# Optimization experiments

Measured on AMD Instinct MI355X. Metric: run time of the kernel, lower is better.

The kernel has to match this reference:

```python
import jax, jax.numpy as jnp
import numpy as np

N, M, E, D = 20000, 1024, 640000, 256


def setup_inputs() -> dict:
    key = jax.random.key(0)
    ks = jax.random.split(key, 24)
    mask = jax.random.uniform(ks[0], (N, M)) < 0.05
    init = jnp.where(mask, jax.random.uniform(ks[1], (N, M), minval=0.1, maxval=1.0), 0.0)
    inp = {
        'init': init,
        'ei_cc': jax.random.randint(ks[2], (2, E), 0, N, dtype=jnp.int32),
        'ei_cac': jax.random.randint(ks[3], (2, E), 0, N, dtype=jnp.int32),
        'ei_csc': jax.random.randint(ks[4], (2, E), 0, N, dtype=jnp.int32),
        'ea_cc': jax.random.uniform(ks[5], (E,), minval=0.1, maxval=1.0),
        'ea_cac': jax.random.uniform(ks[6], (E,), minval=0.1, maxval=1.0),
        'ea_csc': jax.random.uniform(ks[7], (E,), minval=0.1, maxval=1.0),
        # Projection MLP: Linear(1,16) -> ReLU -> Linear(16,D)
        'pW1': jax.random.normal(ks[8], (1, 16)) * 0.5,
        'pb1': jnp.zeros((16,)),
        'pW2': jax.random.normal(ks[9], (16, D)) * 0.1,
        'pb2': jnp.zeros((D,)),
        # three GCN branches, 3 layers each (all D->D)
        'W_cc': jax.random.normal(ks[10], (3, D, D)) * 0.05,
        'b_cc': jnp.zeros((3, D)),
        'W_cac': jax.random.normal(ks[11], (3, D, D)) * 0.05,
        'b_cac': jnp.zeros((3, D)),
        'W_csc': jax.random.normal(ks[12], (3, D, D)) * 0.05,
        'b_csc': jnp.zeros((3, D)),
        # meta-path attention: Linear(D, 1)
        'w_att': jax.random.normal(ks[13], (D,)) * 0.05,
        'b_att': jnp.zeros((1,)),
    }
    return inp


def projection(init, pW1, pb1, pW2, pb2):
    # torch code feeds the *indices* of nonzero columns through the MLP and
    # mean-pools per row. Vectorize: precompute MLP(j) for every column index j,
    # then masked mean.
    idx = jnp.arange(M, dtype=init.dtype)[:, None]          # [M, 1]
    h = jax.nn.relu(idx @ pW1 + pb1)                        # [M, 16]
    col_emb = h @ pW2 + pb2                                 # [M, D]
    mask = (init != 0).astype(init.dtype)                   # [N, M]
    cnt = mask.sum(axis=1)                                  # [N]
    emb = (mask @ col_emb) / jnp.maximum(cnt, 1.0)[:, None]
    return jnp.where(cnt[:, None] > 0, emb, 0.0)            # zero rows stay zero


def gcn_conv(x, edge_index, edge_weight, W, b):
    # PyG GCNConv with edge_weight: add self loops (w=1), symmetric norm.
    n = x.shape[0]
    loop = jnp.arange(n, dtype=edge_index.dtype)
    row = jnp.concatenate([edge_index[0], loop])
    col = jnp.concatenate([edge_index[1], loop])
    w = jnp.concatenate([edge_weight, jnp.ones((n,), x.dtype)])
    deg = jax.ops.segment_sum(w, col, num_segments=n)
    dinv = jnp.where(deg > 0, jax.lax.rsqrt(deg), 0.0)
    norm = dinv[row] * w * dinv[col]                        # [E+N]
    h = x @ W                                               # [N, D]
    out = jax.ops.segment_sum(norm[:, None] * h[row], col, num_segments=n)
    return out + b


def gcn_branch(x, edge_index, edge_weight, Ws, bs):
    for l in range(3):
        x = jax.nn.relu(gcn_conv(x, edge_index, edge_weight, Ws[l], bs[l]))
    return x


def reference(init, ei_cc, ei_cac, ei_csc, ea_cc, ea_cac, ea_csc,
              pW1, pb1, pW2, pb2, W_cc, b_cc, W_cac, b_cac, W_csc, b_csc,
              w_att, b_att):
    x0 = projection(init, pW1, pb1, pW2, pb2)               # [N, D]
    out_cc = gcn_branch(x0, ei_cc, ea_cc, W_cc, b_cc)
    out_cac = gcn_branch(x0, ei_cac, ea_cac, W_cac, b_cac)
    out_csc = gcn_branch(x0, ei_csc, ea_csc, W_csc, b_csc)
    emb = jnp.stack([out_cc, out_cac, out_csc], axis=0)     # [3, N, D]
    scores = jnp.einsum('pnd,d->pn', emb, w_att) + b_att[0] # [3, N]
    attn = jax.nn.softmax(scores, axis=0)                   # softmax over meta-paths
    return jnp.einsum('pn,pnd->nd', attn, emb)              # [N, D]
```

## Files before the change

### kernel.cpp

```cpp
#include <hip/hip_runtime.h>
#include <hip/hip_bf16.h>

typedef __hip_bfloat16 bf16;
typedef __bf16 v8bf __attribute__((ext_vector_type(8)));
typedef float f32x4 __attribute__((ext_vector_type(4)));

constexpr int N = 20000, M = 1024, E = 640000, D = 256;
constexpr size_t SEGEL = (size_t)N * D;
constexpr int NCHUNK = 10000;
constexpr int NSLICE = 64;
constexpr int ESLICE = E / NSLICE;

__device__ __forceinline__ float b2f(bf16 v) { return __bfloat162float(v); }
__device__ __forceinline__ bf16 f2b(float f) { return __float2bfloat16(f); }
__device__ __forceinline__ float u2f(unsigned short u) { return __uint_as_float(((unsigned)u) << 16); }
__device__ __forceinline__ unsigned short f2u(float f) { bf16 h = __float2bfloat16(f); return *(unsigned short*)&h; }
__device__ __forceinline__ float loadf(const void* p, size_t i, int isbf) {
    return isbf ? b2f(((const bf16*)p)[i]) : ((const float*)p)[i];
}
__device__ __forceinline__ void fma8(float* acc, uint4 v, float w) {
    acc[0] = fmaf(w, u2f((unsigned short)(v.x & 0xffffu)), acc[0]);
    acc[1] = fmaf(w, u2f((unsigned short)(v.x >> 16)), acc[1]);
    acc[2] = fmaf(w, u2f((unsigned short)(v.y & 0xffffu)), acc[2]);
    acc[3] = fmaf(w, u2f((unsigned short)(v.y >> 16)), acc[3]);
    acc[4] = fmaf(w, u2f((unsigned short)(v.z & 0xffffu)), acc[4]);
    acc[5] = fmaf(w, u2f((unsigned short)(v.z >> 16)), acc[5]);
    acc[6] = fmaf(w, u2f((unsigned short)(v.w & 0xffffu)), acc[6]);
    acc[7] = fmaf(w, u2f((unsigned short)(v.w >> 16)), acc[7]);
}
__device__ __forceinline__ void add4(float* acc, uint2 v) {
    acc[0] += u2f((unsigned short)(v.x & 0xffffu));
    acc[1] += u2f((unsigned short)(v.x >> 16));
    acc[2] += u2f((unsigned short)(v.y & 0xffffu));
    acc[3] += u2f((unsigned short)(v.y >> 16));
}
__device__ __forceinline__ unsigned pack2(float a, float b) {
    return (unsigned)f2u(a) | ((unsigned)f2u(b) << 16);
}

__global__ void detect_kernel(const void* __restrict__ ea, int* __restrict__ flag)
{
    if (threadIdx.x == 0 && blockIdx.x == 0) {
        const unsigned short* u = (const unsigned short*)ea;
        int cnt = 0;
        for (int i = 0; i < 64; i++) {
            float f = __uint_as_float(((unsigned)u[i]) << 16);
            if (f >= 0.05f && f <= 1.05f) cnt++;
        }
        *flag = (cnt >= 60) ? 1 : 0;
    }
}

__global__ __launch_bounds__(256) void transpose_kernel(
    const void* __restrict__ W0, const void* __restrict__ W1, const void* __restrict__ W2,
    bf16* __restrict__ WT, const int* __restrict__ flag)
{
    int isbf = *flag;
    int b = blockIdx.x;
    int mat = b >> 8, n = b & 255, k = threadIdx.x;
    const void* W = (mat < 3) ? W0 : (mat < 6) ? W1 : W2;
    int lm = mat - (mat < 3 ? 0 : (mat < 6 ? 3 : 6));
    WT[(size_t)mat * 65536 + n * 256 + k] =
        f2b(loadf(W, (size_t)lm * 65536 + k * 256 + n, isbf));
}

__global__ __launch_bounds__(256) void cemb_kernel(
    const void* __restrict__ pW1, const void* __restrict__ pb1,
    const void* __restrict__ pW2, const void* __restrict__ pb2,
    bf16* __restrict__ cemb, const int* __restrict__ flag)
{
    int isbf = *flag;
    int j = blockIdx.x;
    int d = threadIdx.x;
    float jf = (float)j;
    float acc = loadf(pb2, d, isbf);
    #pragma unroll
    for (int k = 0; k < 16; k++) {
        float h = fmaxf(jf * loadf(pW1, k, isbf) + loadf(pb1, k, isbf), 0.0f);
        acc += h * loadf(pW2, k * 256 + d, isbf);
    }
    cemb[(size_t)j * 256 + d] = f2b(acc);
}

__global__ __launch_bounds__(256) void projection_kernel(
    const void* __restrict__ init, const bf16* __restrict__ cemb,
    bf16* __restrict__ x0, const int* __restrict__ flag)
{
    __shared__ unsigned short idxs[4][1024];
    int isbf = *flag;
    int wave = threadIdx.x >> 6, lane = threadIdx.x & 63;
    int i = blockIdx.x * 4 + wave;
    unsigned long long below = (lane == 63) ? 0x7fffffffffffffffull
                                            : ((1ull << lane) - 1ull);
    int cnt = 0;
    if (isbf) {
        const unsigned short* row = (const unsigned short*)init + (size_t)i * 1024;
        for (int c0 = 0; c0 < 1024; c0 += 64) {
            bool nz = (row[c0 + lane] & 0x7fffu) != 0;
            unsigned long long m = __ballot(nz);
            if (nz) idxs[wave][cnt + __popcll(m & below)] = (unsigned short)(c0 + lane);
            cnt += __popcll(m);
        }
    } else {
        const float* row = (const float*)init + (size_t)i * 1024;
        for (int c0 = 0; c0 < 1024; c0 += 64) {
            bool nz = row[c0 + lane] != 0.0f;
            unsigned long long m = __ballot(nz);
            if (nz) idxs[wave][cnt + __popcll(m & below)] = (unsigned short)(c0 + lane);
            cnt += __popcll(m);
        }
    }
    const uint2* cr = (const uint2*)cemb;
    float acc[4] = {0.0f, 0.0f, 0.0f, 0.0f};
    int j = 0;
    for (; j + 4 <= cnt; j += 4) {
        int ca = idxs[wave][j], cb = idxs[wave][j + 1];
        int cc = idxs[wave][j + 2], cd = idxs[wave][j + 3];
        uint2 va = cr[(size_t)ca * 64 + lane];
        uint2 vb = cr[(size_t)cb * 64 + lane];
        uint2 vc = cr[(size_t)cc * 64 + lane];
        uint2 vd = cr[(size_t)cd * 64 + lane];
        add4(acc, va); add4(acc, vb); add4(acc, vc); add4(acc, vd);
    }
    for (; j < cnt; j++) {
        uint2 v = cr[(size_t)idxs[wave][j] * 64 + lane];
        add4(acc, v);
    }
    float rinv = 1.0f / fmaxf((float)cnt, 1.0f);
    uint2 o;
    o.x = pack2(acc[0] * rinv, acc[1] * rinv);
    o.y = pack2(acc[2] * rinv, acc[3] * rinv);
    ((uint2*)x0)[(size_t)i * 64 + lane] = o;
}

__global__ __launch_bounds__(256) void countP_kernel(
    const int* __restrict__ e0, const int* __restrict__ e1, const int* __restrict__ e2,
    int* __restrict__ P)
{
    __shared__ int cur[NCHUNK];
    int b = blockIdx.x;
    int pb = b >> 7, rem = b & 127;
    int ck = rem >> 6, s = rem & 63;
    const int* ei = pb == 0 ? e0 : pb == 1 ? e1 : e2;
    int c0 = ck * NCHUNK;
    int t = threadIdx.x;
    for (int i = t; i < NCHUNK; i += 256) cur[i] = 0;
    __syncthreads();
    int ebase = s * ESLICE;
    for (int e = ebase + t; e < ebase + ESLICE; e += 256) {
        int c = ei[E + e];
        if (c >= c0 && c < c0 + NCHUNK) atomicAdd(&cur[c - c0], 1);
    }
    __syncthreads();
    int* Prow = P + ((size_t)(pb * NSLICE + s)) * N + c0;
    for (int i = t; i < NCHUNK; i += 256) Prow[i] = cur[i];
}

__global__ __launch_bounds__(256) void cnt_sum_kernel(
    const int* __restrict__ P, int* __restrict__ cnt)
{
    int id = blockIdx.x * 256 + threadIdx.x;
    if (id >= 3 * N) return;
    int pb = id / N, c = id - pb * N;
    int sum = 0;
    #pragma unroll 8
    for (int s = 0; s < NSLICE; s++)
        sum += P[((size_t)(pb * NSLICE + s)) * N + c];
    cnt[id] = sum;
}

__global__ __launch_bounds__(1024) void scan_kernel(
    const int* __restrict__ cnt, int* __restrict__ col_ptr)
{
    int pb = blockIdx.x;
    int base = pb * E;
    __shared__ int s[1024];
    int t = threadIdx.x;
    const int CH = 20;
    int i0 = t * CH;
    int sum = 0;
    for (int j = 0; j < CH; j++) { int i = i0 + j; if (i < N) sum += cnt[pb * N + i]; }
    s[t] = sum;
    __syncthreads();
    for (int off = 1; off < 1024; off <<= 1) {
        int v = (t >= off) ? s[t - off] : 0;
        __syncthreads();
        s[t] += v;
        __syncthreads();
    }
    int run = base + s[t] - sum;
    for (int j = 0; j < CH; j++) {
        int i = i0 + j;
        if (i < N) {
            col_ptr[pb * (N + 1) + i] = run;
            run += cnt[pb * N + i];
        }
    }
    if (t == 0) col_ptr[pb * (N + 1) + N] = base + E;
}

__global__ __launch_bounds__(256) void base_kernel(
    int* __restrict__ P, const int* __restrict__ col_ptr)
{
    int id = blockIdx.x * 256 + threadIdx.x;
    if (id >= 3 * N) return;
    int pb = id / N, c = id - pb * N;
    int run = col_ptr[pb * (N + 1) + c];
    for (int s = 0; s < NSLICE; s++) {
        size_t idx = ((size_t)(pb * NSLICE + s)) * N + c;
        int v = P[idx];
        P[idx] = run;
        run += v;
    }
}

__global__ __launch_bounds__(256) void fill_kernel(
    const int* __restrict__ e0, const int* __restrict__ e1, const int* __restrict__ e2,
    const void* __restrict__ a0, const void* __restrict__ a1, const void* __restrict__ a2,
    const int* __restrict__ P, int2* __restrict__ epack, const int* __restrict__ flag)
{
    __shared__ int cur[NCHUNK];
    int isbf = *flag;
    int b = blockIdx.x;
    int pb = b >> 7, rem = b & 127;
    int ck = rem >> 6, s = rem & 63;
    const int* ei = pb == 0 ? e0 : pb == 1 ? e1 : e2;
    const void* ea = pb == 0 ? a0 : pb == 1 ? a1 : a2;
    int c0 = ck * NCHUNK;
    int t = threadIdx.x;
    const int* Prow = P + ((size_t)(pb * NSLICE + s)) * N + c0;
    for (int i = t; i < NCHUNK; i += 256) cur[i] = Prow[i];
    __syncthreads();
    int ebase = s * ESLICE;
    for (int e = ebase + t; e < ebase + ESLICE; e += 256) {
        int c = ei[E + e];
        if (c >= c0 && c < c0 + NCHUNK) {
            int r = ei[e];
            float w = loadf(ea, e, isbf);
            int pos = atomicAdd(&cur[c - c0], 1);
            int2 v; v.x = r; v.y = __float_as_int(w);
            epack[pos] = v;
        }
    }
}

__global__ __launch_bounds__(256) void degsum_kernel(
    const int* __restrict__ col_ptr, const int2* __restrict__ epack,
    float* __restrict__ dinv, float* __restrict__ nloop)
{
    int wave = threadIdx.x >> 6, lane = threadIdx.x & 63;
    int pb = blockIdx.x / 5000;
    int i = (blockIdx.x - pb * 5000) * 4 + wave;
    int start = col_ptr[pb * (N + 1) + i], end = col_ptr[pb * (N + 1) + i + 1];
    float sum = 0.0f;
    for (int p = start + lane; p < end; p += 64) sum += __int_as_float(epack[p].y);
    for (int off = 1; off < 64; off <<= 1) sum += __shfl_xor(sum, off, 64);
    if (lane == 0) {
        float dg = 1.0f + sum;
        dinv[pb * N + i] = rsqrtf(dg);
        nloop[pb * N + i] = 1.0f / dg;
    }
}

__global__ __launch_bounds__(256) void snorm_kernel(
    const int* __restrict__ col_ptr, int2* __restrict__ epack,
    const float* __restrict__ dinv)
{
    int wave = threadIdx.x >> 6, lane = threadIdx.x & 63;
    int pb = blockIdx.x / 5000;
    int i = (blockIdx.x - pb * 5000) * 4 + wave;
    int start = col_ptr[pb * (N + 1) + i], end = col_ptr[pb * (N + 1) + i + 1];
    float dc = dinv[pb * N + i];
    for (int p = start + lane; p < end; p += 64) {
        int2 v = epack[p];
        epack[p].y = __float_as_int(dc * __int_as_float(v.y) * dinv[pb * N + v.x]);
    }
}

__global__ __launch_bounds__(256) void aggregate_kernel(
    const bf16* __restrict__ xi0, const bf16* __restrict__ xi1, const bf16* __restrict__ xi2,
    bf16* __restrict__ yb,
    const int* __restrict__ col_ptr, const int2* __restrict__ epack,
    const float* __restrict__ nloop)
{
    int wave = threadIdx.x >> 6, lane = threadIdx.x & 63;
    int pb = blockIdx.x / 5000;
    int i = (blockIdx.x - pb * 5000) * 4 + wave;
    const bf16* x = pb == 0 ? xi0 : pb == 1 ? xi1 : xi2;
    const uint4* xr = (const uint4*)x;
    int L = lane & 31, h = lane >> 5;
    int start = col_ptr[pb * (N + 1) + i], end = col_ptr[pb * (N + 1) + i + 1];
    float nl = nloop[pb * N + i];
    float acc[8];
    {
        uint4 sv = xr[(size_t)i * 32 + L];
        float self = (h == 0) ? nl : 0.0f;
        #pragma unroll
        for (int j = 0; j < 8; j++) acc[j] = 0.0f;
        fma8(acc, sv, self);
    }
    for (int base = start; base < end; base += 64) {
        int n = end - base; n = n < 64 ? n : 64;
        int2 ep; ep.x = 0; ep.y = 0;
        if (lane < n) ep = epack[base + lane];
        #pragma unroll 8
        for (int jj = 0; jj < n; jj += 2) {
            int rj = __shfl(ep.x, jj + h, 64);
            float wj = __int_as_float(__shfl(ep.y, jj + h, 64));
            uint4 v = xr[(size_t)rj * 32 + L];
            fma8(acc, v, wj);
        }
    }
    #pragma unroll
    for (int j = 0; j < 8; j++) acc[j] += __shfl_xor(acc[j], 32, 64);
    if (h == 0) {
        uint4 o;
        o.x = pack2(acc[0], acc[1]);
        o.y = pack2(acc[2], acc[3]);
        o.z = pack2(acc[4], acc[5]);
        o.w = pack2(acc[6], acc[7]);
        ((uint4*)yb)[(size_t)pb * (SEGEL / 8) + (size_t)i * 32 + L] = o;
    }
}

__global__ __launch_bounds__(256) void gemm_relu_kernel(
    const bf16* __restrict__ yb, const bf16* __restrict__ WT, int layer,
    const void* __restrict__ b0, const void* __restrict__ b1, const void* __restrict__ b2,
    bf16* __restrict__ o0, bf16* __restrict__ o1, bf16* __restrict__ o2,
    const int* __restrict__ flag)
{
    int isbf = *flag;
    int pl = blockIdx.x / 1250;
    int rem = blockIdx.x - pl * 1250;
    int mblk = rem >> 1, nh = rem & 1;
    const bf16* y = yb + (size_t)pl * SEGEL;
    const bf16* wt = WT + (size_t)(pl * 3 + layer) * 65536;
    const void* bias = pl == 0 ? b0 : pl == 1 ? b1 : b2;
    bf16* xout = pl == 0 ? o0 : pl == 1 ? o1 : o2;

    int wave = threadIdx.x >> 6, lane = threadIdx.x & 63;
    int m0 = mblk * 32 + (wave >> 1) * 16;
    int n0 = nh * 128 + (wave & 1) * 64;
    int mrow = lane & 15, q = lane >> 4;

    f32x4 acc[4] = {};
    const v8bf* arow = reinterpret_cast<const v8bf*>(y + (size_t)(m0 + mrow) * 256);
    for (int k0 = 0; k0 < 256; k0 += 32) {
        v8bf a = arow[(k0 >> 3) + q];
        #pragma unroll
        for (int nt = 0; nt < 4; nt++) {
            const v8bf* brow = reinterpret_cast<const v8bf*>(wt + (size_t)(n0 + nt * 16 + mrow) * 256);
            acc[nt] = __builtin_amdgcn_mfma_f32_16x16x32_bf16(a, brow[(k0 >> 3) + q], acc[nt], 0, 0, 0);
        }
    }
    #pragma unroll
    for (int nt = 0; nt < 4; nt++) {
        int col = n0 + nt * 16 + mrow;
        float bv = loadf(bias, (size_t)layer * 256 + col, isbf);
        #pragma unroll
        for (int r = 0; r < 4; r++) {
            int row = m0 + q * 4 + r;
            xout[(size_t)row * 256 + col] = f2b(fmaxf(acc[nt][r] + bv, 0.0f));
        }
    }
}

__global__ __launch_bounds__(256) void attention_kernel(
    const bf16* __restrict__ e0, const bf16* __restrict__ e1, const bf16* __restrict__ e2,
    const void* __restrict__ w_att, void* __restrict__ out, int n_nodes,
    const int* __restrict__ flag)
{
    int isbf = *flag;
    int wave = threadIdx.x >> 6, lane = threadIdx.x & 63;
    int n = blockIdx.x * 4 + wave;
    if (n >= n_nodes) return;
    int d0 = lane * 4;
    float w[4], v0[4], v1[4], v2[4];
    #pragma unroll
    for (int j = 0; j < 4; j++) {
        w[j]  = loadf(w_att, d0 + j, isbf);
        v0[j] = b2f(e0[(size_t)n * 256 + d0 + j]);
        v1[j] = b2f(e1[(size_t)n * 256 + d0 + j]);
        v2[j] = b2f(e2[(size_t)n * 256 + d0 + j]);
    }
    float s0 = 0, s1 = 0, s2 = 0;
    #pragma unroll
    for (int j = 0; j < 4; j++) { s0 += v0[j] * w[j]; s1 += v1[j] * w[j]; s2 += v2[j] * w[j]; }
    for (int off = 1; off < 64; off <<= 1) {
        s0 += __shfl_xor(s0, off, 64);
        s1 += __shfl_xor(s1, off, 64);
        s2 += __shfl_xor(s2, off, 64);
    }
    float m = fmaxf(s0, fmaxf(s1, s2));
    float a0 = expf(s0 - m), a1 = expf(s1 - m), a2 = expf(s2 - m);
    float inv = 1.0f / (a0 + a1 + a2);
    a0 *= inv; a1 *= inv; a2 *= inv;
    #pragma unroll
    for (int j = 0; j < 4; j++) {
        float v = a0 * v0[j] + a1 * v1[j] + a2 * v2[j];
        if (isbf) ((bf16*)out)[(size_t)n * 256 + d0 + j] = f2b(v);
        else      ((float*)out)[(size_t)n * 256 + d0 + j] = v;
    }
}

extern "C" void kernel_launch(void* const* d_in, const int* in_sizes, int n_in,
                              void* d_out, int out_size, void* d_ws, size_t ws_size,
                              hipStream_t stream)
{
    (void)in_sizes; (void)n_in; (void)out_size; (void)ws_size;

    const void* init = d_in[0];
    const int*  ei[3] = {(const int*)d_in[1], (const int*)d_in[2], (const int*)d_in[3]};
    const void* ea[3] = {d_in[4], d_in[5], d_in[6]};
    const void* pW1 = d_in[7];
    const void* pb1 = d_in[8];
    const void* pW2 = d_in[9];
    const void* pb2 = d_in[10];
    const void* Wb[3] = {d_in[11], d_in[13], d_in[15]};
    const void* bb[3] = {d_in[12], d_in[14], d_in[16]};
    const void* w_att = d_in[17];

    char* ws = (char*)d_ws;
    size_t off = 0;
    auto carve = [&](size_t bytes) -> char* {
        off = (off + 255) & ~(size_t)255;
        char* p = ws + off; off += bytes; return p;
    };
    int*   flag  = (int*)carve(4);
    bf16*  WT    = (bf16*)carve((size_t)9 * 65536 * 2);
    bf16*  cemb  = (bf16*)carve((size_t)M * D * 2);
    bf16*  x0    = (bf16*)carve(SEGEL * 2);
    int*   cnt   = (int*)carve((size_t)3 * N * 4);
    int*   colp  = (int*)carve((size_t)3 * (N + 1) * 4);
    float* dinv  = (float*)carve((size_t)3 * N * 4);
    float* nloop = (float*)carve((size_t)3 * N * 4);
    int2*  epack = (int2*)carve((size_t)3 * E * 8);
    bf16*  ybuf  = (bf16*)carve((size_t)3 * SEGEL * 2);
    bf16*  bufA  = (bf16*)carve((size_t)3 * SEGEL * 2);
    bf16*  bufB  = (bf16*)carve((size_t)3 * SEGEL * 2);
    int* P = (int*)bufB;

    detect_kernel<<<1, 64, 0, stream>>>(ea[0], flag);
    transpose_kernel<<<2304, 256, 0, stream>>>(Wb[0], Wb[1], Wb[2], WT, flag);
    cemb_kernel<<<M, 256, 0, stream>>>(pW1, pb1, pW2, pb2, cemb, flag);
    projection_kernel<<<5000, 256, 0, stream>>>(init, cemb, x0, flag);

    countP_kernel<<<384, 256, 0, stream>>>(ei[0], ei[1], ei[2], P);
    cnt_sum_kernel<<<(3 * N + 255) / 256, 256, 0, stream>>>(P, cnt);
    scan_kernel<<<3, 1024, 0, stream>>>(cnt, colp);
    base_kernel<<<(3 * N + 255) / 256, 256, 0, stream>>>(P, colp);
    fill_kernel<<<384, 256, 0, stream>>>(ei[0], ei[1], ei[2], ea[0], ea[1], ea[2],
                                         P, epack, flag);
    degsum_kernel<<<15000, 256, 0, stream>>>(colp, epack, dinv, nloop);
    snorm_kernel<<<15000, 256, 0, stream>>>(colp, epack, dinv);

    const bf16 *i0 = x0, *i1 = x0, *i2 = x0;
    bf16* dsts[3] = {bufA, bufB, bufA};
    for (int l = 0; l < 3; l++) {
        aggregate_kernel<<<15000, 256, 0, stream>>>(i0, i1, i2, ybuf, colp, epack, nloop);
        bf16* dst = dsts[l];
        gemm_relu_kernel<<<3750, 256, 0, stream>>>(ybuf, WT, l, bb[0], bb[1], bb[2],
                                                   dst, dst + SEGEL, dst + 2 * SEGEL, flag);
        i0 = dst; i1 = dst + SEGEL; i2 = dst + 2 * SEGEL;
    }
    attention_kernel<<<5000, 256, 0, stream>>>(bufA, bufA + SEGEL, bufA + 2 * SEGEL,
                                               w_att, d_out, N, flag);
}
```

Before: 898.4 us.

## Map GCN branches to XCD groups and use nontemporal edge/output accesses

Block indices are remapped so that each GCN branch runs on a fixed subset of the eight XCDs (3/3/2), which keeps each branch's feature matrix resident in its own XCDs' L2 during the gather-heavy aggregation. Edge-list loads and aggregated-output stores switch to nontemporal hints so they do not evict the reused feature rows. The GEMM kernel now computes all 256 output columns per block (8 MFMA tiles per wave instead of 4), halving the number of A-tile reloads. The trade-offs are uneven load (branch 2 gets fewer XCDs, so its blocks run with less parallelism), some launched blocks that exit immediately, and higher register pressure in the GEMM.

```diff
diff --git a/kernel.cpp b/kernel.cpp
--- a/kernel.cpp
+++ b/kernel.cpp
@@ -4,6 +4,7 @@
 typedef __hip_bfloat16 bf16;
 typedef __bf16 v8bf __attribute__((ext_vector_type(8)));
 typedef float f32x4 __attribute__((ext_vector_type(4)));
+typedef unsigned int v4u __attribute__((ext_vector_type(4)));
 
 constexpr int N = 20000, M = 1024, E = 640000, D = 256;
 constexpr size_t SEGEL = (size_t)N * D;
@@ -36,6 +37,14 @@
 }
 __device__ __forceinline__ unsigned pack2(float a, float b) {
     return (unsigned)f2u(a) | ((unsigned)f2u(b) << 16);
+}
+__device__ __forceinline__ void xcd_branch(int bid, int per_branch, int& pb, int& nb) {
+    int x8 = bid & 7, s = bid >> 3;
+    pb = (x8 < 3) ? 0 : (x8 < 6) ? 1 : 2;
+    int rank = x8 - (pb == 0 ? 0 : pb == 1 ? 3 : 6);
+    int gsz = (pb == 2) ? 2 : 3;
+    nb = s * gsz + rank;
+    if (nb >= per_branch) nb = -1;
 }
 
 __global__ void detect_kernel(const void* __restrict__ ea, int* __restrict__ flag)
@@ -284,8 +293,10 @@
     const float* __restrict__ nloop)
 {
     int wave = threadIdx.x >> 6, lane = threadIdx.x & 63;
-    int pb = blockIdx.x / 5000;
-    int i = (blockIdx.x - pb * 5000) * 4 + wave;
+    int pb, nb;
+    xcd_branch(blockIdx.x, 5000, pb, nb);
+    if (nb < 0) return;
+    int i = nb * 4 + wave;
     const bf16* x = pb == 0 ? xi0 : pb == 1 ? xi1 : xi2;
     const uint4* xr = (const uint4*)x;
     int L = lane & 31, h = lane >> 5;
@@ -301,12 +312,17 @@
     }
     for (int base = start; base < end; base += 64) {
         int n = end - base; n = n < 64 ? n : 64;
-        int2 ep; ep.x = 0; ep.y = 0;
-        if (lane < n) ep = epack[base + lane];
+        int ex = 0, ey = 0;
+        if (lane < n) {
+            unsigned long long ev = __builtin_nontemporal_load(
+                (const unsigned long long*)(epack + base + lane));
+            ex = (int)(unsigned)(ev & 0xffffffffull);
+            ey = (int)(unsigned)(ev >> 32);
+        }
         #pragma unroll 8
         for (int jj = 0; jj < n; jj += 2) {
-            int rj = __shfl(ep.x, jj + h, 64);
-            float wj = __int_as_float(__shfl(ep.y, jj + h, 64));
+            int rj = __shfl(ex, jj + h, 64);
+            float wj = __int_as_float(__shfl(ey, jj + h, 64));
             uint4 v = xr[(size_t)rj * 32 + L];
             fma8(acc, v, wj);
         }
@@ -314,12 +330,13 @@
     #pragma unroll
     for (int j = 0; j < 8; j++) acc[j] += __shfl_xor(acc[j], 32, 64);
     if (h == 0) {
-        uint4 o;
+        v4u o;
         o.x = pack2(acc[0], acc[1]);
         o.y = pack2(acc[2], acc[3]);
         o.z = pack2(acc[4], acc[5]);
         o.w = pack2(acc[6], acc[7]);
-        ((uint4*)yb)[(size_t)pb * (SEGEL / 8) + (size_t)i * 32 + L] = o;
+        __builtin_nontemporal_store(o,
+            (v4u*)yb + (size_t)pb * (SEGEL / 8) + (size_t)i * 32 + L);
     }
 }
 
@@ -330,31 +347,31 @@
     const int* __restrict__ flag)
 {
     int isbf = *flag;
-    int pl = blockIdx.x / 1250;
-    int rem = blockIdx.x - pl * 1250;
-    int mblk = rem >> 1, nh = rem & 1;
+    int pl, blk;
+    xcd_branch(blockIdx.x, 625, pl, blk);
+    if (blk < 0) return;
     const bf16* y = yb + (size_t)pl * SEGEL;
     const bf16* wt = WT + (size_t)(pl * 3 + layer) * 65536;
     const void* bias = pl == 0 ? b0 : pl == 1 ? b1 : b2;
     bf16* xout = pl == 0 ? o0 : pl == 1 ? o1 : o2;
 
     int wave = threadIdx.x >> 6, lane = threadIdx.x & 63;
-    int m0 = mblk * 32 + (wave >> 1) * 16;
-    int n0 = nh * 128 + (wave & 1) * 64;
+    int m0 = blk * 32 + (wave >> 1) * 16;
+    int n0 = (wave & 1) * 128;
     int mrow = lane & 15, q = lane >> 4;
 
-    f32x4 acc[4] = {};
+    f32x4 acc[8] = {};
     const v8bf* arow = reinterpret_cast<const v8bf*>(y + (size_t)(m0 + mrow) * 256);
     for (int k0 = 0; k0 < 256; k0 += 32) {
         v8bf a = arow[(k0 >> 3) + q];
         #pragma unroll
-        for (int nt = 0; nt < 4; nt++) {
+        for (int nt = 0; nt < 8; nt++) {
             const v8bf* brow = reinterpret_cast<const v8bf*>(wt + (size_t)(n0 + nt * 16 + mrow) * 256);
             acc[nt] = __builtin_amdgcn_mfma_f32_16x16x32_bf16(a, brow[(k0 >> 3) + q], acc[nt], 0, 0, 0);
         }
     }
     #pragma unroll
-    for (int nt = 0; nt < 4; nt++) {
+    for (int nt = 0; nt < 8; nt++) {
         int col = n0 + nt * 16 + mrow;
         float bv = loadf(bias, (size_t)layer * 256 + col, isbf);
         #pragma unroll
@@ -457,9 +474,9 @@
     const bf16 *i0 = x0, *i1 = x0, *i2 = x0;
     bf16* dsts[3] = {bufA, bufB, bufA};
     for (int l = 0; l < 3; l++) {
-        aggregate_kernel<<<15000, 256, 0, stream>>>(i0, i1, i2, ybuf, colp, epack, nloop);
+        aggregate_kernel<<<20000, 256, 0, stream>>>(i0, i1, i2, ybuf, colp, epack, nloop);
         bf16* dst = dsts[l];
-        gemm_relu_kernel<<<3750, 256, 0, stream>>>(ybuf, WT, l, bb[0], bb[1], bb[2],
+        gemm_relu_kernel<<<2504, 256, 0, stream>>>(ybuf, WT, l, bb[0], bb[1], bb[2],
                                                    dst, dst + SEGEL, dst + 2 * SEGEL, flag);
         i0 = dst; i1 = dst + SEGEL; i2 = dst + 2 * SEGEL;
     }
```

After: 1.024 ms. 1.14x slower.

## Fuse sparse aggregation and dense GEMM+ReLU into one kernel via LDS tile

Applied to the files above, without the earlier changes.

Merges the per-layer aggregate and gemm_relu kernels into a single kernel. Each block aggregates 32 destination rows into a shared-memory tile, then runs the MFMA GEMM with bias and ReLU directly from that tile. This removes the round trip of the intermediate aggregated buffer through global memory and one launch per layer. In exchange the grid shrinks from 15000 to 1875 blocks, each wave processes 8 rows serially, and the whole block waits at a barrier before the GEMM, which can hurt latency hiding for the gather-bound phase.

```diff
diff --git a/kernel.cpp b/kernel.cpp
--- a/kernel.cpp
+++ b/kernel.cpp
@@ -277,90 +277,84 @@
     }
 }
 
-__global__ __launch_bounds__(256) void aggregate_kernel(
+__global__ __launch_bounds__(256) void agg_gemm_kernel(
     const bf16* __restrict__ xi0, const bf16* __restrict__ xi1, const bf16* __restrict__ xi2,
-    bf16* __restrict__ yb,
+    const bf16* __restrict__ WT, int layer,
+    const void* __restrict__ b0, const void* __restrict__ b1, const void* __restrict__ b2,
+    bf16* __restrict__ o0, bf16* __restrict__ o1, bf16* __restrict__ o2,
     const int* __restrict__ col_ptr, const int2* __restrict__ epack,
-    const float* __restrict__ nloop)
-{
-    int wave = threadIdx.x >> 6, lane = threadIdx.x & 63;
-    int pb = blockIdx.x / 5000;
-    int i = (blockIdx.x - pb * 5000) * 4 + wave;
+    const float* __restrict__ nloop, const int* __restrict__ flag)
+{
+    __shared__ unsigned short ytile[32][264];
+    int isbf = *flag;
+    int pb = blockIdx.x / 625;
+    int m0 = (blockIdx.x - pb * 625) * 32;
     const bf16* x = pb == 0 ? xi0 : pb == 1 ? xi1 : xi2;
     const uint4* xr = (const uint4*)x;
+    int wave = threadIdx.x >> 6, lane = threadIdx.x & 63;
     int L = lane & 31, h = lane >> 5;
-    int start = col_ptr[pb * (N + 1) + i], end = col_ptr[pb * (N + 1) + i + 1];
-    float nl = nloop[pb * N + i];
-    float acc[8];
-    {
-        uint4 sv = xr[(size_t)i * 32 + L];
-        float self = (h == 0) ? nl : 0.0f;
+
+    for (int k = 0; k < 8; k++) {
+        int i = m0 + wave * 8 + k;
+        int start = col_ptr[pb * (N + 1) + i], end = col_ptr[pb * (N + 1) + i + 1];
+        float nl = nloop[pb * N + i];
+        float acc[8];
+        {
+            uint4 sv = xr[(size_t)i * 32 + L];
+            float self = (h == 0) ? nl : 0.0f;
+            #pragma unroll
+            for (int j = 0; j < 8; j++) acc[j] = 0.0f;
+            fma8(acc, sv, self);
+        }
+        for (int base = start; base < end; base += 64) {
+            int n = end - base; n = n < 64 ? n : 64;
+            int ex = 0, ey = 0;
+            if (lane < n) { int2 ep = epack[base + lane]; ex = ep.x; ey = ep.y; }
+            #pragma unroll 8
+            for (int jj = 0; jj < n; jj += 2) {
+                int rj = __shfl(ex, jj + h, 64);
+                float wj = __int_as_float(__shfl(ey, jj + h, 64));
+                uint4 v = xr[(size_t)rj * 32 + L];
+                fma8(acc, v, wj);
+            }
+        }
         #pragma unroll
-        for (int j = 0; j < 8; j++) acc[j] = 0.0f;
-        fma8(acc, sv, self);
-    }
-    for (int base = start; base < end; base += 64) {
-        int n = end - base; n = n < 64 ? n : 64;
-        int2 ep; ep.x = 0; ep.y = 0;
-        if (lane < n) ep = epack[base + lane];
-        #pragma unroll 8
-        for (int jj = 0; jj < n; jj += 2) {
-            int rj = __shfl(ep.x, jj + h, 64);
-            float wj = __int_as_float(__shfl(ep.y, jj + h, 64));
-            uint4 v = xr[(size_t)rj * 32 + L];
-            fma8(acc, v, wj);
+        for (int j = 0; j < 8; j++) acc[j] += __shfl_xor(acc[j], 32, 64);
+        if (h == 0) {
+            uint4 o;
+            o.x = pack2(acc[0], acc[1]);
+            o.y = pack2(acc[2], acc[3]);
+            o.z = pack2(acc[4], acc[5]);
+            o.w = pack2(acc[6], acc[7]);
+            *(uint4*)&ytile[wave * 8 + k][L * 8] = o;
+        }
+    }
+    __syncthreads();
+
+    const bf16* wt = WT + (size_t)(pb * 3 + layer) * 65536;
+    const void* bias = pb == 0 ? b0 : pb == 1 ? b1 : b2;
+    bf16* xout = pb == 0 ? o0 : pb == 1 ? o1 : o2;
+    int mh = wave >> 1, nh = wave & 1;
+    int mrow = lane & 15, q = lane >> 4;
+
+    f32x4 acc2[8] = {};
+    for (int k0 = 0; k0 < 256; k0 += 32) {
+        v8bf a = *(const v8bf*)&ytile[mh * 16 + mrow][k0 + q * 8];
+        #pragma unroll
+        for (int nt = 0; nt < 8; nt++) {
+            const v8bf* brow = reinterpret_cast<const v8bf*>(
+                wt + (size_t)(nh * 128 + nt * 16 + mrow) * 256);
+            acc2[nt] = __builtin_amdgcn_mfma_f32_16x16x32_bf16(a, brow[(k0 >> 3) + q], acc2[nt], 0, 0, 0);
         }
     }
     #pragma unroll
-    for (int j = 0; j < 8; j++) acc[j] += __shfl_xor(acc[j], 32, 64);
-    if (h == 0) {
-        uint4 o;
-        o.x = pack2(acc[0], acc[1]);
-        o.y = pack2(acc[2], acc[3]);
-        o.z = pack2(acc[4], acc[5]);
-        o.w = pack2(acc[6], acc[7]);
-        ((uint4*)yb)[(size_t)pb * (SEGEL / 8) + (size_t)i * 32 + L] = o;
-    }
-}
-
-__global__ __launch_bounds__(256) void gemm_relu_kernel(
-    const bf16* __restrict__ yb, const bf16* __restrict__ WT, int layer,
-    const void* __restrict__ b0, const void* __restrict__ b1, const void* __restrict__ b2,
-    bf16* __restrict__ o0, bf16* __restrict__ o1, bf16* __restrict__ o2,
-    const int* __restrict__ flag)
-{
-    int isbf = *flag;
-    int pl = blockIdx.x / 1250;
-    int rem = blockIdx.x - pl * 1250;
-    int mblk = rem >> 1, nh = rem & 1;
-    const bf16* y = yb + (size_t)pl * SEGEL;
-    const bf16* wt = WT + (size_t)(pl * 3 + layer) * 65536;
-    const void* bias = pl == 0 ? b0 : pl == 1 ? b1 : b2;
-    bf16* xout = pl == 0 ? o0 : pl == 1 ? o1 : o2;
-
-    int wave = threadIdx.x >> 6, lane = threadIdx.x & 63;
-    int m0 = mblk * 32 + (wave >> 1) * 16;
-    int n0 = nh * 128 + (wave & 1) * 64;
-    int mrow = lane & 15, q = lane >> 4;
-
-    f32x4 acc[4] = {};
-    const v8bf* arow = reinterpret_cast<const v8bf*>(y + (size_t)(m0 + mrow) * 256);
-    for (int k0 = 0; k0 < 256; k0 += 32) {
-        v8bf a = arow[(k0 >> 3) + q];
-        #pragma unroll
-        for (int nt = 0; nt < 4; nt++) {
-            const v8bf* brow = reinterpret_cast<const v8bf*>(wt + (size_t)(n0 + nt * 16 + mrow) * 256);
-            acc[nt] = __builtin_amdgcn_mfma_f32_16x16x32_bf16(a, brow[(k0 >> 3) + q], acc[nt], 0, 0, 0);
-        }
-    }
-    #pragma unroll
-    for (int nt = 0; nt < 4; nt++) {
-        int col = n0 + nt * 16 + mrow;
+    for (int nt = 0; nt < 8; nt++) {
+        int col = nh * 128 + nt * 16 + mrow;
         float bv = loadf(bias, (size_t)layer * 256 + col, isbf);
         #pragma unroll
         for (int r = 0; r < 4; r++) {
-            int row = m0 + q * 4 + r;
-            xout[(size_t)row * 256 + col] = f2b(fmaxf(acc[nt][r] + bv, 0.0f));
+            int row = m0 + mh * 16 + q * 4 + r;
+            xout[(size_t)row * 256 + col] = f2b(fmaxf(acc2[nt][r] + bv, 0.0f));
         }
     }
 }
@@ -435,7 +429,6 @@
     float* dinv  = (float*)carve((size_t)3 * N * 4);
     float* nloop = (float*)carve((size_t)3 * N * 4);
     int2*  epack = (int2*)carve((size_t)3 * E * 8);
-    bf16*  ybuf  = (bf16*)carve((size_t)3 * SEGEL * 2);
     bf16*  bufA  = (bf16*)carve((size_t)3 * SEGEL * 2);
     bf16*  bufB  = (bf16*)carve((size_t)3 * SEGEL * 2);
     int* P = (int*)bufB;
@@ -457,10 +450,10 @@
     const bf16 *i0 = x0, *i1 = x0, *i2 = x0;
     bf16* dsts[3] = {bufA, bufB, bufA};
     for (int l = 0; l < 3; l++) {
-        aggregate_kernel<<<15000, 256, 0, stream>>>(i0, i1, i2, ybuf, colp, epack, nloop);
         bf16* dst = dsts[l];
-        gemm_relu_kernel<<<3750, 256, 0, stream>>>(ybuf, WT, l, bb[0], bb[1], bb[2],
-                                                   dst, dst + SEGEL, dst + 2 * SEGEL, flag);
+        agg_gemm_kernel<<<1875, 256, 0, stream>>>(
+            i0, i1, i2, WT, l, bb[0], bb[1], bb[2],
+            dst, dst + SEGEL, dst + 2 * SEGEL, colp, epack, nloop, flag);
         i0 = dst; i1 = dst + SEGEL; i2 = dst + 2 * SEGEL;
     }
     attention_kernel<<<5000, 256, 0, stream>>>(bufA, bufA + SEGEL, bufA + 2 * SEGEL,
```

Result: slower. 953.9 us (+6.2%).

## Sort CSC edge chunks by source row and widen GEMM tile to full N

Applied to the files above, without the earlier changes.

The normalization kernel now bitonic-sorts each 64-edge chunk of every destination's edge list by source index, using wave shuffles, while writing the normalized weights. The goal is more locality in the aggregate gathers of source rows across the three layers. Separately, the GEMM kernel now gives each wave all 128 columns of its half instead of 64, halving the block count so the A-row loads are reused across twice as many MFMA tiles. The trade-offs are a more expensive one-time sort pass and higher register pressure in the GEMM.

```diff
diff --git a/kernel.cpp b/kernel.cpp
--- a/kernel.cpp
+++ b/kernel.cpp
@@ -262,7 +262,7 @@
     }
 }
 
-__global__ __launch_bounds__(256) void snorm_kernel(
+__global__ __launch_bounds__(256) void snorm_sort_kernel(
     const int* __restrict__ col_ptr, int2* __restrict__ epack,
     const float* __restrict__ dinv)
 {
@@ -271,9 +271,31 @@
     int i = (blockIdx.x - pb * 5000) * 4 + wave;
     int start = col_ptr[pb * (N + 1) + i], end = col_ptr[pb * (N + 1) + i + 1];
     float dc = dinv[pb * N + i];
-    for (int p = start + lane; p < end; p += 64) {
-        int2 v = epack[p];
-        epack[p].y = __float_as_int(dc * __int_as_float(v.y) * dinv[pb * N + v.x]);
+    for (int base = start; base < end; base += 64) {
+        int n = end - base; n = n < 64 ? n : 64;
+        int key = 0x7fffffff, val = 0;
+        if (lane < n) {
+            int2 v = epack[base + lane];
+            key = v.x;
+            val = __float_as_int(dc * __int_as_float(v.y) * dinv[pb * N + v.x]);
+        }
+        #pragma unroll
+        for (int k = 2; k <= 64; k <<= 1) {
+            #pragma unroll
+            for (int j = k >> 1; j > 0; j >>= 1) {
+                int pk = __shfl_xor(key, j, 64);
+                int pv = __shfl_xor(val, j, 64);
+                bool up = (lane & k) == 0;
+                bool lower = (lane & j) == 0;
+                bool takeMin = (up == lower);
+                bool sw = takeMin ? (pk < key) : (pk > key);
+                if (sw) { key = pk; val = pv; }
+            }
+        }
+        if (lane < n) {
+            int2 o; o.x = key; o.y = val;
+            epack[base + lane] = o;
+        }
     }
 }
 
@@ -301,12 +323,12 @@
     }
     for (int base = start; base < end; base += 64) {
         int n = end - base; n = n < 64 ? n : 64;
-        int2 ep; ep.x = 0; ep.y = 0;
-        if (lane < n) ep = epack[base + lane];
+        int ex = 0, ey = 0;
+        if (lane < n) { int2 ep = epack[base + lane]; ex = ep.x; ey = ep.y; }
         #pragma unroll 8
         for (int jj = 0; jj < n; jj += 2) {
-            int rj = __shfl(ep.x, jj + h, 64);
-            float wj = __int_as_float(__shfl(ep.y, jj + h, 64));
+            int rj = __shfl(ex, jj + h, 64);
+            float wj = __int_as_float(__shfl(ey, jj + h, 64));
             uint4 v = xr[(size_t)rj * 32 + L];
             fma8(acc, v, wj);
         }
@@ -330,31 +352,29 @@
     const int* __restrict__ flag)
 {
     int isbf = *flag;
-    int pl = blockIdx.x / 1250;
-    int rem = blockIdx.x - pl * 1250;
-    int mblk = rem >> 1, nh = rem & 1;
+    int pl = blockIdx.x / 625, blk = blockIdx.x - pl * 625;
     const bf16* y = yb + (size_t)pl * SEGEL;
     const bf16* wt = WT + (size_t)(pl * 3 + layer) * 65536;
     const void* bias = pl == 0 ? b0 : pl == 1 ? b1 : b2;
     bf16* xout = pl == 0 ? o0 : pl == 1 ? o1 : o2;
 
     int wave = threadIdx.x >> 6, lane = threadIdx.x & 63;
-    int m0 = mblk * 32 + (wave >> 1) * 16;
-    int n0 = nh * 128 + (wave & 1) * 64;
+    int m0 = blk * 32 + (wave >> 1) * 16;
+    int n0 = (wave & 1) * 128;
     int mrow = lane & 15, q = lane >> 4;
 
-    f32x4 acc[4] = {};
+    f32x4 acc[8] = {};
     const v8bf* arow = reinterpret_cast<const v8bf*>(y + (size_t)(m0 + mrow) * 256);
     for (int k0 = 0; k0 < 256; k0 += 32) {
         v8bf a = arow[(k0 >> 3) + q];
         #pragma unroll
-        for (int nt = 0; nt < 4; nt++) {
+        for (int nt = 0; nt < 8; nt++) {
             const v8bf* brow = reinterpret_cast<const v8bf*>(wt + (size_t)(n0 + nt * 16 + mrow) * 256);
             acc[nt] = __builtin_amdgcn_mfma_f32_16x16x32_bf16(a, brow[(k0 >> 3) + q], acc[nt], 0, 0, 0);
         }
     }
     #pragma unroll
-    for (int nt = 0; nt < 4; nt++) {
+    for (int nt = 0; nt < 8; nt++) {
         int col = n0 + nt * 16 + mrow;
         float bv = loadf(bias, (size_t)layer * 256 + col, isbf);
         #pragma unroll
@@ -452,14 +472,14 @@
     fill_kernel<<<384, 256, 0, stream>>>(ei[0], ei[1], ei[2], ea[0], ea[1], ea[2],
                                          P, epack, flag);
     degsum_kernel<<<15000, 256, 0, stream>>>(colp, epack, dinv, nloop);
-    snorm_kernel<<<15000, 256, 0, stream>>>(colp, epack, dinv);
+    snorm_sort_kernel<<<15000, 256, 0, stream>>>(colp, epack, dinv);
 
     const bf16 *i0 = x0, *i1 = x0, *i2 = x0;
     bf16* dsts[3] = {bufA, bufB, bufA};
     for (int l = 0; l < 3; l++) {
         aggregate_kernel<<<15000, 256, 0, stream>>>(i0, i1, i2, ybuf, colp, epack, nloop);
         bf16* dst = dsts[l];
-        gemm_relu_kernel<<<3750, 256, 0, stream>>>(ybuf, WT, l, bb[0], bb[1], bb[2],
+        gemm_relu_kernel<<<1875, 256, 0, stream>>>(ybuf, WT, l, bb[0], bb[1], bb[2],
                                                    dst, dst + SEGEL, dst + 2 * SEGEL, flag);
         i0 = dst; i1 = dst + SEGEL; i2 = dst + 2 * SEGEL;
     }
```

New measurement: 897.9 us. No clear change (-0.1%).
